# Optimization experiments

Hardware: AMD Instinct MI355X
Metric: run time of the kernel (lower is better)

The kernel has to match this reference:

```python
import jax, jax.numpy as jnp
import numpy as np

B, O, N = 8, 100, 4096
TOK_D, D, K, H = 2048, 256, 128, 8
DH = D // H
LN_EPS = 1e-5


def _ln(x, g, b):
    m = x.mean(-1, keepdims=True)
    v = ((x - m) ** 2).mean(-1, keepdims=True)
    return (x - m) * jax.lax.rsqrt(v + LN_EPS) * g + b


def setup_inputs() -> dict:
    key = jax.random.key(0)
    ks = jax.random.split(key, 16)
    s = 0.02
    return {
        "activation": jax.random.uniform(ks[0], (B, O, N), jnp.float32),
        "tokens": jax.random.normal(ks[1], (B, N, TOK_D), jnp.float32),
        "W_tok": jax.random.normal(ks[2], (TOK_D, D), jnp.float32) * s,
        "b_tok": jnp.zeros((D,), jnp.float32),
        "g_tn": jnp.ones((D,), jnp.float32),
        "bt_tn": jnp.zeros((D,), jnp.float32),
        "pool_query": jax.random.normal(ks[3], (D,), jnp.float32) * s,
        "Wq": jax.random.normal(ks[4], (D, D), jnp.float32) * s,
        "bq": jnp.zeros((D,), jnp.float32),
        "Wk": jax.random.normal(ks[5], (D, D), jnp.float32) * s,
        "bk": jnp.zeros((D,), jnp.float32),
        "Wv": jax.random.normal(ks[6], (D, D), jnp.float32) * s,
        "bv": jnp.zeros((D,), jnp.float32),
        "Wo": jax.random.normal(ks[7], (D, D), jnp.float32) * s,
        "bo": jnp.zeros((D,), jnp.float32),
        "g_pn": jnp.ones((D,), jnp.float32),
        "bt_pn": jnp.zeros((D,), jnp.float32),
        "g_on": jnp.ones((D,), jnp.float32),
        "bt_on": jnp.zeros((D,), jnp.float32),
    }


def reference(activation, tokens, W_tok, b_tok, g_tn, bt_tn, pool_query,
              Wq, bq, Wk, bk, Wv, bv, Wo, bo, g_pn, bt_pn, g_on, bt_on):
    # project + norm the shared token pool: [B, N, D]
    tp = _ln(tokens @ W_tok + b_tok, g_tn, bt_tn)

    # weighted-average branch
    w = activation / jnp.clip(activation.sum(-1, keepdims=True), 1e-8)
    weighted_avg = jnp.einsum('bon,bnd->bod', w, tp)

    # top-k attention branch
    _, topk_idx = jax.lax.top_k(activation, K)            # [B, O, K]
    topk_tokens = jax.vmap(lambda t, i: t[i])(tp, topk_idx)  # [B, O, K, D]

    # MultiheadAttention with a single shared query vector (q_len = 1)
    q = (pool_query @ Wq + bq).reshape(H, DH)             # [H, DH]
    kp = (topk_tokens @ Wk + bk).reshape(B, O, K, H, DH)
    vp = (topk_tokens @ Wv + bv).reshape(B, O, K, H, DH)
    scores = jnp.einsum('hd,bokhd->bohk', q, kp) / np.sqrt(DH).astype(np.float32)
    attn = jax.nn.softmax(scores, axis=-1)                # [B, O, H, K]
    pooled = jnp.einsum('bohk,bokhd->bohd', attn, vp).reshape(B, O, D)
    pooled = _ln(pooled @ Wo + bo, g_pn, bt_pn)

    return _ln(weighted_avg + pooled, g_on, bt_on)
```

## Files before the change

### kernel.cpp

```cpp
#include <hip/hip_runtime.h>
#include <hip/hip_bf16.h>

#define DEVI static __device__ __forceinline__

typedef __attribute__((ext_vector_type(8))) short short8;
typedef __attribute__((ext_vector_type(4))) float f32x4;

#define B_   8
#define O_   100
#define N_   4096
#define TOKD 2048
#define D_   256
#define K_   128
#define H_   8
#define M_   (B_*N_)

DEVI unsigned short f2bf(float f) {
    unsigned u = __float_as_uint(f);
    u = (u + 0x7FFFu + ((u >> 16) & 1u)) >> 16;
    return (unsigned short)u;
}
DEVI float bf2f(unsigned v) { return __uint_as_float(v << 16); }

DEVI unsigned pkbf(float lo, float hi) {
    unsigned r;
    asm("v_cvt_pk_bf16_f32 %0, %1, %2" : "=v"(r) : "v"(lo), "v"(hi));
    return r;
}
DEVI void gload16(const void* g, void* l) {
    __builtin_amdgcn_global_load_lds((const __attribute__((address_space(1))) void*)g,
                                     (__attribute__((address_space(3))) void*)l, 16, 0, 0);
}

__global__ __launch_bounds__(256) void k_trans(const float* __restrict__ W,
                                               unsigned short* __restrict__ wtb) {
    __shared__ unsigned short ldsT[32 * 264];
    const int t = threadIdx.x;
    const int k0 = (blockIdx.x >> 3) * 256;
    const int n0 = (blockIdx.x & 7) * 32;
    const int nn = t & 31, kk8 = t >> 5;
    #pragma unroll
    for (int r = 0; r < 32; ++r) {
        int k = r * 8 + kk8;
        ldsT[nn * 264 + k] = f2bf(W[(size_t)(k0 + k) * D_ + n0 + nn]);
    }
    __syncthreads();
    const int w = t >> 6, l = t & 63;
    #pragma unroll
    for (int rr = 0; rr < 8; ++rr) {
        int n = w * 8 + rr;
        ushort4 v = *(const ushort4*)(&ldsT[n * 264 + l * 4]);
        *(ushort4*)(wtb + (size_t)(n0 + n) * TOKD + k0 + l * 4) = v;
    }
}

__global__ __launch_bounds__(256) void k_topkqf(const float* __restrict__ act,
                                                int* __restrict__ oidx,
                                                float* __restrict__ asum,
                                                const float* __restrict__ pq,
                                                const float* __restrict__ Wq,
                                                const float* __restrict__ bqv,
                                                const float* __restrict__ Wk,
                                                const float* __restrict__ bkv,
                                                float* __restrict__ qW,
                                                float* __restrict__ qb) {
    __shared__ __align__(16) char smem[50304];
    const int t = threadIdx.x, lane = t & 63, wid = t >> 6;

    if (blockIdx.x >= 800) {
        float (*qpart)[32] = (float(*)[32])smem;
        float* qhl = (float*)(smem + 1024);
        const int h = blockIdx.x - 800;
        const int col = h * 32 + (t & 31), sl = t >> 5;
        float s = 0.f;
        #pragma unroll
        for (int e = 0; e < 32; ++e) s += pq[sl * 32 + e] * Wq[(sl * 32 + e) * D_ + col];
        qpart[sl][t & 31] = s;
        __syncthreads();
        if (t < 32) {
            float u = bqv[h * 32 + t];
            #pragma unroll
            for (int s8 = 0; s8 < 8; ++s8) u += qpart[s8][t];
            qhl[t] = u;
        }
        __syncthreads();
        float u = 0.f;
        #pragma unroll
        for (int dd = 0; dd < 32; ++dd) u += qhl[dd] * Wk[t * D_ + h * 32 + dd];
        qW[h * D_ + t] = u;
        if (t == 0) {
            float z = 0.f;
            for (int dd = 0; dd < 32; ++dd) z += qhl[dd] * bkv[h * 32 + dd];
            qb[h] = z;
        }
        return;
    }

    int* hist = (int*)smem;
    unsigned long long* cand = (unsigned long long*)(smem + 16384);
    int* csum = (int*)(smem + 49152);
    int* sb   = (int*)(smem + 50192);
    int* cnts = (int*)(smem + 50200);
    float* redf = (float*)(smem + 50208);
    unsigned long long* redu = (unsigned long long*)(smem + 50224);

    const int blk = blockIdx.x;
    const float* rp = act + (size_t)blk * N_;
    float fv[16]; unsigned vb[16]; int bins[16];
    float fs = 0.f;
    #pragma unroll
    for (int i = 0; i < 16; ++i) {
        float f = rp[t + i * 256];
        fv[i] = f; vb[i] = __float_as_uint(f);
        fs += f;
    }
    #pragma unroll
    for (int i = 0; i < 16; ++i) hist[t + i * 256] = 0;
    if (t == 0) { cnts[0] = 0; cnts[1] = 0; }
    #pragma unroll
    for (int m = 1; m < 64; m <<= 1) fs += __shfl_xor(fs, m);
    if (!lane) redf[wid] = fs;
    __syncthreads();
    if (t == 0) asum[blk] = fmaxf(redf[0] + redf[1] + redf[2] + redf[3], 1e-8f);

    #pragma unroll
    for (int i = 0; i < 16; ++i) {
        float f = fv[i];
        int b = (f >= 1.0f) ? 4095 : ((f > 0.f) ? (int)(f * 4096.f) : 0);
        bins[i] = b;
        atomicAdd(&hist[b], 1);
    }
    __syncthreads();

    int cs = 0;
    #pragma unroll
    for (int i = 0; i < 16; ++i) cs += hist[t * 16 + i];
    int v = cs;
    #pragma unroll
    for (int off = 1; off < 64; off <<= 1) {
        int o = __shfl_down(v, off);
        if (lane + off < 64) v += o;
    }
    if (!lane) csum[256 + wid] = v;
    __syncthreads();
    int stot = 0;
    for (int w2 = wid + 1; w2 < 4; ++w2) stot += csum[256 + w2];
    int suff = v + stot;
    csum[t] = suff;
    __syncthreads();
    int nxtc = (t < 255) ? csum[t + 1] : 0;
    if (suff >= K_ && nxtc < K_) {
        int run = nxtc, bstar = t * 16;
        for (int bi = 15; bi >= 0; --bi) {
            run += hist[t * 16 + bi];
            if (run >= K_) { bstar = t * 16 + bi; break; }
        }
        sb[0] = bstar;
    }
    __syncthreads();
    const int bstar = sb[0];

    #pragma unroll
    for (int i = 0; i < 16; ++i) {
        if (bins[i] > bstar) {
            int p = atomicAdd(&cnts[0], 1);
            oidx[blk * K_ + p] = t + i * 256;
        } else if (bins[i] == bstar) {
            int p = atomicAdd(&cnts[1], 1);
            cand[p] = ((unsigned long long)vb[i] << 16) | (unsigned)(4095 - (t + i * 256));
        }
    }
    __syncthreads();
    const int g = cnts[0], E = cnts[1], m = K_ - g;
    unsigned long long last = ~0ull;
    for (int slot = 0; slot < m; ++slot) {
        unsigned long long best = 0;
        for (int i = t; i < E; i += 256) {
            unsigned long long e = cand[i];
            if (e < last && e > best) best = e;
        }
        #pragma unroll
        for (int mm = 1; mm < 64; mm <<= 1) {
            unsigned long long o = __shfl_xor(best, mm);
            if (o > best) best = o;
        }
        if (!lane) redu[wid] = best;
        __syncthreads();
        best = redu[0];
        if (redu[1] > best) best = redu[1];
        if (redu[2] > best) best = redu[2];
        if (redu[3] > best) best = redu[3];
        if (t == 0) oidx[blk * K_ + g + slot] = 4095 - (int)(best & 0xFFFFull);
        last = best;
        __syncthreads();
    }
}

__global__ __launch_bounds__(512, 2) void k_gemm1(const float* __restrict__ A,
                                                  const unsigned short* __restrict__ Bt,
                                                  const float* __restrict__ btok,
                                                  const float* __restrict__ g,
                                                  const float* __restrict__ bt,
                                                  unsigned short* __restrict__ tp) {
    __shared__ __align__(16) char smem[81920];
    const int t = threadIdx.x;
    const int bm = blockIdx.x;
    const int lane = t & 63, w = t >> 6;
    const int wm = w >> 2, wn = w & 3;
    const int lr = lane >> 4, lc = lane & 15;

    const int arow = t >> 3;
    const int acb = (t & 7) * 16;
    const float* agp = A + (size_t)(bm * 64 + arow) * TOKD + (t & 7) * 8;
    const int aw0 = arow * 128 + (acb ^ ((arow & 7) << 4));
    const unsigned short* bg = Bt + (size_t)(t >> 3) * TOKD
                        + (((((t & 7) << 4)) ^ (((t >> 3) & 7) << 4)) >> 1);
    char* bld = smem + 16384 + (w << 10);

    f32x4 acc[2][4] = {};
    const int NT = TOKD / 64;
    float4 a0, a1;

    a0 = *(const float4*)(agp); a1 = *(const float4*)(agp + 4);
    #pragma unroll
    for (int c = 0; c < 4; ++c) gload16(bg + (size_t)c * 64 * TOKD, bld + c * 8192);
    {
        uint4 v;
        v.x = pkbf(a0.x, a0.y); v.y = pkbf(a0.z, a0.w);
        v.z = pkbf(a1.x, a1.y); v.w = pkbf(a1.z, a1.w);
        *(uint4*)(smem + aw0) = v;
    }
    a0 = *(const float4*)(agp + 64); a1 = *(const float4*)(agp + 68);
    asm volatile("s_waitcnt vmcnt(2) lgkmcnt(0)" ::: "memory");
    __builtin_amdgcn_s_barrier();

    int cur = 0;
    for (int kt = 0; kt < NT; ++kt) {
        const int nxt = cur ^ 1;
        if (kt + 1 < NT) {
            const unsigned short* bn = bg + (size_t)(kt + 1) * 64;
            char* dst = bld + nxt * 32768;
            #pragma unroll
            for (int c = 0; c < 4; ++c) gload16(bn + (size_t)c * 64 * TOKD, dst + c * 8192);
        }
        const char* Ab = smem + cur * 8192;
        const char* Bb = smem + 16384 + cur * 32768;
        #pragma unroll
        for (int kk = 0; kk < 2; ++kk) {
            short8 afr[2], bfr[4];
            #pragma unroll
            for (int mi = 0; mi < 2; ++mi) {
                int row = wm * 32 + mi * 16 + lc;
                afr[mi] = *(const short8*)(Ab + row * 128 + ((kk * 64 + lr * 16) ^ ((row & 7) << 4)));
            }
            #pragma unroll
            for (int ni = 0; ni < 4; ++ni) {
                int n = wn * 64 + ni * 16 + lc;
                bfr[ni] = *(const short8*)(Bb + n * 128 + ((kk * 64 + lr * 16) ^ ((n & 7) << 4)));
            }
            __builtin_amdgcn_s_setprio(1);
            #pragma unroll
            for (int mi = 0; mi < 2; ++mi)
                #pragma unroll
                for (int ni = 0; ni < 4; ++ni)
                    acc[mi][ni] = __builtin_amdgcn_mfma_f32_16x16x32_bf16(afr[mi], bfr[ni], acc[mi][ni], 0, 0, 0);
            __builtin_amdgcn_s_setprio(0);
        }
        if (kt + 1 < NT) {
            uint4 v;
            v.x = pkbf(a0.x, a0.y); v.y = pkbf(a0.z, a0.w);
            v.z = pkbf(a1.x, a1.y); v.w = pkbf(a1.z, a1.w);
            *(uint4*)(smem + nxt * 8192 + aw0) = v;
            if (kt + 2 < NT) {
                const float* ap = agp + (size_t)(kt + 2) * 64;
                a0 = *(const float4*)(ap); a1 = *(const float4*)(ap + 4);
                asm volatile("s_waitcnt vmcnt(2) lgkmcnt(0)" ::: "memory");
            } else {
                asm volatile("s_waitcnt vmcnt(0) lgkmcnt(0)" ::: "memory");
            }
            __builtin_amdgcn_s_barrier();
            cur = nxt;
        }
    }
    __syncthreads();

    float* ep = (float*)smem;
    const int col0 = lane * 4;
    float4 b4 = *(const float4*)(btok + col0);
    float4 g4 = *(const float4*)(g + col0);
    float4 t4 = *(const float4*)(bt + col0);
    #pragma unroll
    for (int c = 0; c < 2; ++c) {
        if (wm == c) {
            #pragma unroll
            for (int mi = 0; mi < 2; ++mi)
                #pragma unroll
                for (int ni = 0; ni < 4; ++ni)
                    #pragma unroll
                    for (int r = 0; r < 4; ++r)
                        ep[(mi * 16 + lr * 4 + r) * 260 + wn * 64 + ni * 16 + lc] = acc[mi][ni][r];
        }
        __syncthreads();
        #pragma unroll
        for (int rr = 0; rr < 4; ++rr) {
            int row = w * 4 + rr;
            float4 x4 = *(const float4*)(ep + row * 260 + col0);
            float x0 = x4.x + b4.x, x1 = x4.y + b4.y, x2 = x4.z + b4.z, x3 = x4.w + b4.w;
            float s = x0 + x1 + x2 + x3;
            float q = x0*x0 + x1*x1 + x2*x2 + x3*x3;
            #pragma unroll
            for (int m = 1; m < 64; m <<= 1) { s += __shfl_xor(s, m); q += __shfl_xor(q, m); }
            float mean = s * (1.f/256.f);
            float var = q * (1.f/256.f) - mean * mean;
            float rs = rsqrtf(var + 1e-5f);
            ushort4 o;
            o.x = f2bf((x0-mean)*rs*g4.x + t4.x);
            o.y = f2bf((x1-mean)*rs*g4.y + t4.y);
            o.z = f2bf((x2-mean)*rs*g4.z + t4.z);
            o.w = f2bf((x3-mean)*rs*g4.w + t4.w);
            *(ushort4*)(tp + (size_t)(bm * 64 + c * 32 + row) * D_ + col0) = o;
        }
        __syncthreads();
    }
}

__global__ __launch_bounds__(256) void k_wavg(const float* __restrict__ act,
                                              const unsigned short* __restrict__ tp,
                                              float* __restrict__ partial) {
    const int kc = blockIdx.x;
    const int b = blockIdx.y;
    const int d = threadIdx.x;
    const unsigned short* tpb = tp + ((size_t)b * N_ + kc * 128) * D_ + d;
    const float* actb = act + (size_t)b * O_ * N_ + kc * 128;
    float* pout = partial + ((size_t)(b * 32 + kc) * O_) * D_ + d;
    for (int oci = 0; oci < 2; ++oci) {
        const int oc = blockIdx.z * 2 + oci;
        float acc[10] = {};
        #pragma unroll 2
        for (int q = 0; q < 32; ++q) {
            float t0 = bf2f(tpb[(q * 4 + 0) * D_]);
            float t1 = bf2f(tpb[(q * 4 + 1) * D_]);
            float t2 = bf2f(tpb[(q * 4 + 2) * D_]);
            float t3 = bf2f(tpb[(q * 4 + 3) * D_]);
            #pragma unroll
            for (int oj = 0; oj < 10; ++oj) {
                float4 a4 = *(const float4*)(actb + (size_t)(oc * 10 + oj) * N_ + q * 4);
                acc[oj] += a4.x * t0 + a4.y * t1 + a4.z * t2 + a4.w * t3;
            }
        }
        #pragma unroll
        for (int oj = 0; oj < 10; ++oj)
            pout[(size_t)(oc * 10 + oj) * D_] = acc[oj];
    }
}

DEVI int swz64(int j, int chunk) { return j * 512 + ((chunk ^ (j & 31)) << 4); }

__global__ __launch_bounds__(256) void k_attn(
    const unsigned short* __restrict__ tp, const int* __restrict__ oidx,
    const float* __restrict__ qW, const float* __restrict__ qbv,
    const float* __restrict__ Wv, const float* __restrict__ bv,
    const float* __restrict__ Wo, const float* __restrict__ bo,
    const float* __restrict__ g_pn, const float* __restrict__ bt_pn,
    const float* __restrict__ g_on, const float* __restrict__ bt_on,
    const float* __restrict__ partial, const float* __restrict__ asum,
    float* __restrict__ outp)
{
    __shared__ __align__(16) char tg[32768];
    __shared__ float sc[H_ * K_];
    __shared__ float redf[8];
    __shared__ int idxl[K_];
    float* ul = (float*)tg;
    float* pool_lds = (float*)(tg + 8192);

    const int t = threadIdx.x, lane = t & 63, wid = t >> 6;
    const int blk = blockIdx.x;
    const int b = blk / O_;
    const int o = blk - b * O_;

    if (t < K_) idxl[t] = oidx[blk * K_ + t];
    __syncthreads();

    const int jq = t & 63, hp = t >> 6;
    const float* qr0 = qW + (hp * 2) * D_;
    const float* qr1 = qr0 + D_;
    const float sca = 0.1767766952966369f;

    for (int pass = 0; pass < 2; ++pass) {
        #pragma unroll
        for (int it = 0; it < 8; ++it) {
            int c = t + it * 256;
            int j = c >> 5, ch = c & 31;
            uint4 v = *(const uint4*)(tp + ((size_t)(b * N_ + idxl[pass * 64 + j])) * D_ + ch * 8);
            *(uint4*)(tg + swz64(j, ch)) = v;
        }
        __syncthreads();
        float s0 = 0.f, s1 = 0.f;
        #pragma unroll 4
        for (int e8 = 0; e8 < 32; ++e8) {
            uint4 tv = *(const uint4*)(tg + swz64(jq, e8));
            float f0 = bf2f(tv.x & 0xffffu), f1 = bf2f(tv.x >> 16);
            float f2 = bf2f(tv.y & 0xffffu), f3 = bf2f(tv.y >> 16);
            float f4 = bf2f(tv.z & 0xffffu), f5 = bf2f(tv.z >> 16);
            float f6 = bf2f(tv.w & 0xffffu), f7 = bf2f(tv.w >> 16);
            const float* qa = qr0 + e8 * 8;
            const float* qc = qr1 + e8 * 8;
            s0 += f0*qa[0]+f1*qa[1]+f2*qa[2]+f3*qa[3]+f4*qa[4]+f5*qa[5]+f6*qa[6]+f7*qa[7];
            s1 += f0*qc[0]+f1*qc[1]+f2*qc[2]+f3*qc[3]+f4*qc[4]+f5*qc[5]+f6*qc[6]+f7*qc[7];
        }
        sc[(hp * 2)     * K_ + pass * 64 + jq] = (s0 + qbv[hp * 2])     * sca;
        sc[(hp * 2 + 1) * K_ + pass * 64 + jq] = (s1 + qbv[hp * 2 + 1]) * sca;
        __syncthreads();
    }

    #pragma unroll
    for (int hh = 0; hh < 2; ++hh) {
        int h = wid * 2 + hh;
        float v0 = sc[h * K_ + lane], v1 = sc[h * K_ + 64 + lane];
        float mx = fmaxf(v0, v1);
        #pragma unroll
        for (int m = 1; m < 64; m <<= 1) mx = fmaxf(mx, __shfl_xor(mx, m));
        float e0 = __expf(v0 - mx), e1 = __expf(v1 - mx);
        float ss = e0 + e1;
        #pragma unroll
        for (int m = 1; m < 64; m <<= 1) ss += __shfl_xor(ss, m);
        float inv = 1.0f / ss;
        sc[h * K_ + lane] = e0 * inv;
        sc[h * K_ + 64 + lane] = e1 * inv;
    }
    __syncthreads();

    const int hq5 = t >> 5, eg = t & 31;
    float a8[8] = {};
    #pragma unroll 2
    for (int jb = 0; jb < 16; ++jb) {
        f32x4 p4 = *(const f32x4*)(sc + hq5 * K_ + 64 + jb * 4);
        #pragma unroll
        for (int ji = 0; ji < 4; ++ji) {
            int j = jb * 4 + ji;
            uint4 tv = *(const uint4*)(tg + swz64(j, eg));
            float pw = p4[ji];
            a8[0] += pw * bf2f(tv.x & 0xffffu); a8[1] += pw * bf2f(tv.x >> 16);
            a8[2] += pw * bf2f(tv.y & 0xffffu); a8[3] += pw * bf2f(tv.y >> 16);
            a8[4] += pw * bf2f(tv.z & 0xffffu); a8[5] += pw * bf2f(tv.z >> 16);
            a8[6] += pw * bf2f(tv.w & 0xffffu); a8[7] += pw * bf2f(tv.w >> 16);
        }
    }
    __syncthreads();
    #pragma unroll
    for (int it = 0; it < 8; ++it) {
        int c = t + it * 256;
        int j = c >> 5, ch = c & 31;
        uint4 v = *(const uint4*)(tp + ((size_t)(b * N_ + idxl[j])) * D_ + ch * 8);
        *(uint4*)(tg + swz64(j, ch)) = v;
    }
    __syncthreads();
    #pragma unroll 2
    for (int jb = 0; jb < 16; ++jb) {
        f32x4 p4 = *(const f32x4*)(sc + hq5 * K_ + jb * 4);
        #pragma unroll
        for (int ji = 0; ji < 4; ++ji) {
            int j = jb * 4 + ji;
            uint4 tv = *(const uint4*)(tg + swz64(j, eg));
            float pw = p4[ji];
            a8[0] += pw * bf2f(tv.x & 0xffffu); a8[1] += pw * bf2f(tv.x >> 16);
            a8[2] += pw * bf2f(tv.y & 0xffffu); a8[3] += pw * bf2f(tv.y >> 16);
            a8[4] += pw * bf2f(tv.z & 0xffffu); a8[5] += pw * bf2f(tv.z >> 16);
            a8[6] += pw * bf2f(tv.w & 0xffffu); a8[7] += pw * bf2f(tv.w >> 16);
        }
    }
    __syncthreads();
    #pragma unroll
    for (int i = 0; i < 8; ++i) ul[hq5 * D_ + eg * 8 + i] = a8[i];
    __syncthreads();

    {
        int h = t >> 5;
        const float* up = ul + h * D_;
        float p0 = 0.f, p1 = 0.f, p2 = 0.f, p3 = 0.f;
        #pragma unroll 4
        for (int e = 0; e < 64; ++e) {
            p0 += up[e]       * Wv[(size_t)e         * D_ + t];
            p1 += up[e + 64]  * Wv[(size_t)(e + 64)  * D_ + t];
            p2 += up[e + 128] * Wv[(size_t)(e + 128) * D_ + t];
            p3 += up[e + 192] * Wv[(size_t)(e + 192) * D_ + t];
        }
        pool_lds[t] = bv[t] + ((p0 + p1) + (p2 + p3));
    }
    __syncthreads();
    float po;
    {
        float p0 = 0.f, p1 = 0.f, p2 = 0.f, p3 = 0.f;
        #pragma unroll 4
        for (int e = 0; e < 64; ++e) {
            p0 += pool_lds[e]       * Wo[(size_t)e         * D_ + t];
            p1 += pool_lds[e + 64]  * Wo[(size_t)(e + 64)  * D_ + t];
            p2 += pool_lds[e + 128] * Wo[(size_t)(e + 128) * D_ + t];
            p3 += pool_lds[e + 192] * Wo[(size_t)(e + 192) * D_ + t];
        }
        po = bo[t] + ((p0 + p1) + (p2 + p3));
    }

    float lsm = po, lqm = po * po;
    #pragma unroll
    for (int m = 1; m < 64; m <<= 1) { lsm += __shfl_xor(lsm, m); lqm += __shfl_xor(lqm, m); }
    if (!lane) { redf[wid] = lsm; redf[4 + wid] = lqm; }
    __syncthreads();
    lsm = redf[0] + redf[1] + redf[2] + redf[3];
    lqm = redf[4] + redf[5] + redf[6] + redf[7];
    float mean = lsm * (1.f/256.f);
    float var = lqm * (1.f/256.f) - mean * mean;
    float rs = rsqrtf(var + 1e-5f);
    float pl = (po - mean) * rs * g_pn[t] + bt_pn[t];
    __syncthreads();

    float wa = 0.f;
    const float* pp = partial + ((size_t)(b * 32) * O_ + o) * D_ + t;
    #pragma unroll 8
    for (int kc = 0; kc < 32; ++kc) wa += pp[(size_t)kc * O_ * D_];
    float x = wa / asum[blk] + pl;
    float s2 = x, q2 = x * x;
    #pragma unroll
    for (int m = 1; m < 64; m <<= 1) { s2 += __shfl_xor(s2, m); q2 += __shfl_xor(q2, m); }
    if (!lane) { redf[wid] = s2; redf[4 + wid] = q2; }
    __syncthreads();
    s2 = redf[0] + redf[1] + redf[2] + redf[3];
    q2 = redf[4] + redf[5] + redf[6] + redf[7];
    float mean2 = s2 * (1.f/256.f);
    float var2 = q2 * (1.f/256.f) - mean2 * mean2;
    float rs2 = rsqrtf(var2 + 1e-5f);
    outp[(size_t)blk * D_ + t] = (x - mean2) * rs2 * g_on[t] + bt_on[t];
}

extern "C" void kernel_launch(void* const* d_in, const int* in_sizes, int n_in,
                              void* d_out, int out_size, void* d_ws, size_t ws_size,
                              hipStream_t stream) {
    const float* act    = (const float*)d_in[0];
    const float* tokens = (const float*)d_in[1];
    const float* W_tok  = (const float*)d_in[2];
    const float* b_tok  = (const float*)d_in[3];
    const float* g_tn   = (const float*)d_in[4];
    const float* bt_tn  = (const float*)d_in[5];
    const float* pq     = (const float*)d_in[6];
    const float* Wq     = (const float*)d_in[7];
    const float* bq     = (const float*)d_in[8];
    const float* Wk     = (const float*)d_in[9];
    const float* bk     = (const float*)d_in[10];
    const float* Wv     = (const float*)d_in[11];
    const float* bv     = (const float*)d_in[12];
    const float* Wo     = (const float*)d_in[13];
    const float* bo     = (const float*)d_in[14];
    const float* g_pn   = (const float*)d_in[15];
    const float* bt_pn  = (const float*)d_in[16];
    const float* g_on   = (const float*)d_in[17];
    const float* bt_on  = (const float*)d_in[18];

    char* ws = (char*)d_ws;
    unsigned short* wtb   = (unsigned short*)ws;
    unsigned short* tp    = (unsigned short*)(ws + 1048576);
    int*   tidx = (int*)(ws + 17825792);
    float* asum = (float*)(ws + 18235392);
    float* part = (float*)(ws + 18238592);
    float* qW   = (float*)(ws + 44452992);
    float* qb   = (float*)(ws + 44461184);

    k_trans<<<64, 256, 0, stream>>>(W_tok, wtb);
    k_gemm1<<<M_ / 64, 512, 0, stream>>>(tokens, wtb, b_tok, g_tn, bt_tn, tp);
    k_wavg<<<dim3(32, 8, 5), 256, 0, stream>>>(act, tp, part);
    k_topkqf<<<808, 256, 0, stream>>>(act, tidx, asum, pq, Wq, bq, Wk, bk, qW, qb);
    k_attn<<<B_ * O_, 256, 0, stream>>>(tp, tidx, qW, qb, Wv, bv, Wo, bo,
                                        g_pn, bt_pn, g_on, bt_on, part, asum,
                                        (float*)d_out);
}
```

Measured before the change: 219.5 us.

## Shrink token-projection GEMM tile to 32 rows with register-staged loads

The token projection GEMM now uses 32-row M tiles, a K step of 32 and padded unswizzled LDS, so it needs less shared memory and can run more blocks per CU. The direct global-to-LDS loads of W are replaced with register-staged uint4 loads, and only half the threads load A. This targets latency hiding through occupancy and a larger grid. In exchange, each block reuses the full 256-column B tile over fewer rows, so B traffic from L2 doubles and there are twice as many barriers per K.

```diff
diff --git a/kernel.cpp b/kernel.cpp
--- a/kernel.cpp
+++ b/kernel.cpp
@@ -26,10 +26,6 @@
     unsigned r;
     asm("v_cvt_pk_bf16_f32 %0, %1, %2" : "=v"(r) : "v"(lo), "v"(hi));
     return r;
-}
-DEVI void gload16(const void* g, void* l) {
-    __builtin_amdgcn_global_load_lds((const __attribute__((address_space(1))) void*)g,
-                                     (__attribute__((address_space(3))) void*)l, 16, 0, 0);
 }
 
 __global__ __launch_bounds__(256) void k_trans(const float* __restrict__ W,
@@ -196,90 +192,75 @@
     }
 }
 
-__global__ __launch_bounds__(512, 2) void k_gemm1(const float* __restrict__ A,
+__global__ __launch_bounds__(512, 4) void k_gemm1(const float* __restrict__ A,
                                                   const unsigned short* __restrict__ Bt,
                                                   const float* __restrict__ btok,
                                                   const float* __restrict__ g,
                                                   const float* __restrict__ bt,
                                                   unsigned short* __restrict__ tp) {
-    __shared__ __align__(16) char smem[81920];
+    __shared__ __align__(16) char smem[46080];
     const int t = threadIdx.x;
     const int bm = blockIdx.x;
     const int lane = t & 63, w = t >> 6;
     const int wm = w >> 2, wn = w & 3;
     const int lr = lane >> 4, lc = lane & 15;
-
-    const int arow = t >> 3;
-    const int acb = (t & 7) * 16;
-    const float* agp = A + (size_t)(bm * 64 + arow) * TOKD + (t & 7) * 8;
-    const int aw0 = arow * 128 + (acb ^ ((arow & 7) << 4));
-    const unsigned short* bg = Bt + (size_t)(t >> 3) * TOKD
-                        + (((((t & 7) << 4)) ^ (((t >> 3) & 7) << 4)) >> 1);
-    char* bld = smem + 16384 + (w << 10);
-
-    f32x4 acc[2][4] = {};
-    const int NT = TOKD / 64;
-    float4 a0, a1;
-
-    a0 = *(const float4*)(agp); a1 = *(const float4*)(agp + 4);
-    #pragma unroll
-    for (int c = 0; c < 4; ++c) gload16(bg + (size_t)c * 64 * TOKD, bld + c * 8192);
-    {
-        uint4 v;
-        v.x = pkbf(a0.x, a0.y); v.y = pkbf(a0.z, a0.w);
-        v.z = pkbf(a1.x, a1.y); v.w = pkbf(a1.z, a1.w);
-        *(uint4*)(smem + aw0) = v;
-    }
-    a0 = *(const float4*)(agp + 64); a1 = *(const float4*)(agp + 68);
-    asm volatile("s_waitcnt vmcnt(2) lgkmcnt(0)" ::: "memory");
-    __builtin_amdgcn_s_barrier();
-
-    int cur = 0;
+    const int NT = TOKD / 32;
+
+    const bool ast = (t < 256);
+    const float* agp = A + (size_t)(bm * 32 + ((t >> 3) & 31)) * TOKD + (t & 7) * 4;
+    const int awo = (t >> 3) * 80 + (t & 7) * 8;
+    const unsigned short* bgp = Bt + (size_t)(t >> 1) * TOKD + (t & 1) * 16;
+    const int bwo = (t >> 1) * 80 + (t & 1) * 32;
+    const int aro = (wm * 16 + lc) * 80 + lr * 16;
+    const int bro = (wn * 64 + lc) * 80 + lr * 16;
+
+    f32x4 acc[4] = {};
+    float4 ta = {0.f, 0.f, 0.f, 0.f};
+    uint4 tb0, tb1;
+
+    if (ast) ta = *(const float4*)(agp);
+    tb0 = *(const uint4*)(bgp);
+    tb1 = *(const uint4*)(bgp + 8);
+    if (ast) {
+        uint2 v; v.x = pkbf(ta.x, ta.y); v.y = pkbf(ta.z, ta.w);
+        *(uint2*)(smem + awo) = v;
+    }
+    *(uint4*)(smem + 5120 + bwo) = tb0;
+    *(uint4*)(smem + 5120 + bwo + 16) = tb1;
+    if (ast) ta = *(const float4*)(agp + 32);
+    tb0 = *(const uint4*)(bgp + 32);
+    tb1 = *(const uint4*)(bgp + 40);
+    __syncthreads();
+
     for (int kt = 0; kt < NT; ++kt) {
-        const int nxt = cur ^ 1;
+        const int cur = kt & 1, nxt = cur ^ 1;
+        const char* Ab = smem + cur * 2560;
+        const char* Bb = smem + 5120 + cur * 20480;
+        short8 afr = *(const short8*)(Ab + aro);
+        short8 bfr0 = *(const short8*)(Bb + bro);
+        short8 bfr1 = *(const short8*)(Bb + bro + 16 * 80);
+        short8 bfr2 = *(const short8*)(Bb + bro + 32 * 80);
+        short8 bfr3 = *(const short8*)(Bb + bro + 48 * 80);
+        __builtin_amdgcn_s_setprio(1);
+        acc[0] = __builtin_amdgcn_mfma_f32_16x16x32_bf16(afr, bfr0, acc[0], 0, 0, 0);
+        acc[1] = __builtin_amdgcn_mfma_f32_16x16x32_bf16(afr, bfr1, acc[1], 0, 0, 0);
+        acc[2] = __builtin_amdgcn_mfma_f32_16x16x32_bf16(afr, bfr2, acc[2], 0, 0, 0);
+        acc[3] = __builtin_amdgcn_mfma_f32_16x16x32_bf16(afr, bfr3, acc[3], 0, 0, 0);
+        __builtin_amdgcn_s_setprio(0);
         if (kt + 1 < NT) {
-            const unsigned short* bn = bg + (size_t)(kt + 1) * 64;
-            char* dst = bld + nxt * 32768;
-            #pragma unroll
-            for (int c = 0; c < 4; ++c) gload16(bn + (size_t)c * 64 * TOKD, dst + c * 8192);
-        }
-        const char* Ab = smem + cur * 8192;
-        const char* Bb = smem + 16384 + cur * 32768;
-        #pragma unroll
-        for (int kk = 0; kk < 2; ++kk) {
-            short8 afr[2], bfr[4];
-            #pragma unroll
-            for (int mi = 0; mi < 2; ++mi) {
-                int row = wm * 32 + mi * 16 + lc;
-                afr[mi] = *(const short8*)(Ab + row * 128 + ((kk * 64 + lr * 16) ^ ((row & 7) << 4)));
+            if (ast) {
+                uint2 v; v.x = pkbf(ta.x, ta.y); v.y = pkbf(ta.z, ta.w);
+                *(uint2*)(smem + nxt * 2560 + awo) = v;
             }
-            #pragma unroll
-            for (int ni = 0; ni < 4; ++ni) {
-                int n = wn * 64 + ni * 16 + lc;
-                bfr[ni] = *(const short8*)(Bb + n * 128 + ((kk * 64 + lr * 16) ^ ((n & 7) << 4)));
+            *(uint4*)(smem + 5120 + nxt * 20480 + bwo) = tb0;
+            *(uint4*)(smem + 5120 + nxt * 20480 + bwo + 16) = tb1;
+            if (kt + 2 < NT) {
+                if (ast) ta = *(const float4*)(agp + (kt + 2) * 32);
+                tb0 = *(const uint4*)(bgp + (kt + 2) * 32);
+                tb1 = *(const uint4*)(bgp + (kt + 2) * 32 + 8);
             }
-            __builtin_amdgcn_s_setprio(1);
-            #pragma unroll
-            for (int mi = 0; mi < 2; ++mi)
-                #pragma unroll
-                for (int ni = 0; ni < 4; ++ni)
-                    acc[mi][ni] = __builtin_amdgcn_mfma_f32_16x16x32_bf16(afr[mi], bfr[ni], acc[mi][ni], 0, 0, 0);
-            __builtin_amdgcn_s_setprio(0);
-        }
-        if (kt + 1 < NT) {
-            uint4 v;
-            v.x = pkbf(a0.x, a0.y); v.y = pkbf(a0.z, a0.w);
-            v.z = pkbf(a1.x, a1.y); v.w = pkbf(a1.z, a1.w);
-            *(uint4*)(smem + nxt * 8192 + aw0) = v;
-            if (kt + 2 < NT) {
-                const float* ap = agp + (size_t)(kt + 2) * 64;
-                a0 = *(const float4*)(ap); a1 = *(const float4*)(ap + 4);
-                asm volatile("s_waitcnt vmcnt(2) lgkmcnt(0)" ::: "memory");
-            } else {
-                asm volatile("s_waitcnt vmcnt(0) lgkmcnt(0)" ::: "memory");
-            }
+            asm volatile("s_waitcnt lgkmcnt(0)" ::: "memory");
             __builtin_amdgcn_s_barrier();
-            cur = nxt;
         }
     }
     __syncthreads();
@@ -290,37 +271,29 @@
     float4 g4 = *(const float4*)(g + col0);
     float4 t4 = *(const float4*)(bt + col0);
     #pragma unroll
-    for (int c = 0; c < 2; ++c) {
-        if (wm == c) {
-            #pragma unroll
-            for (int mi = 0; mi < 2; ++mi)
-                #pragma unroll
-                for (int ni = 0; ni < 4; ++ni)
-                    #pragma unroll
-                    for (int r = 0; r < 4; ++r)
-                        ep[(mi * 16 + lr * 4 + r) * 260 + wn * 64 + ni * 16 + lc] = acc[mi][ni][r];
-        }
-        __syncthreads();
-        #pragma unroll
-        for (int rr = 0; rr < 4; ++rr) {
-            int row = w * 4 + rr;
-            float4 x4 = *(const float4*)(ep + row * 260 + col0);
-            float x0 = x4.x + b4.x, x1 = x4.y + b4.y, x2 = x4.z + b4.z, x3 = x4.w + b4.w;
-            float s = x0 + x1 + x2 + x3;
-            float q = x0*x0 + x1*x1 + x2*x2 + x3*x3;
-            #pragma unroll
-            for (int m = 1; m < 64; m <<= 1) { s += __shfl_xor(s, m); q += __shfl_xor(q, m); }
-            float mean = s * (1.f/256.f);
-            float var = q * (1.f/256.f) - mean * mean;
-            float rs = rsqrtf(var + 1e-5f);
-            ushort4 o;
-            o.x = f2bf((x0-mean)*rs*g4.x + t4.x);
-            o.y = f2bf((x1-mean)*rs*g4.y + t4.y);
-            o.z = f2bf((x2-mean)*rs*g4.z + t4.z);
-            o.w = f2bf((x3-mean)*rs*g4.w + t4.w);
-            *(ushort4*)(tp + (size_t)(bm * 64 + c * 32 + row) * D_ + col0) = o;
-        }
-        __syncthreads();
+    for (int ni = 0; ni < 4; ++ni)
+        #pragma unroll
+        for (int r = 0; r < 4; ++r)
+            ep[(wm * 16 + lr * 4 + r) * 260 + wn * 64 + ni * 16 + lc] = acc[ni][r];
+    __syncthreads();
+    #pragma unroll
+    for (int rr = 0; rr < 4; ++rr) {
+        int row = w * 4 + rr;
+        float4 x4 = *(const float4*)(ep + row * 260 + col0);
+        float x0 = x4.x + b4.x, x1 = x4.y + b4.y, x2 = x4.z + b4.z, x3 = x4.w + b4.w;
+        float s = x0 + x1 + x2 + x3;
+        float q = x0*x0 + x1*x1 + x2*x2 + x3*x3;
+        #pragma unroll
+        for (int m = 1; m < 64; m <<= 1) { s += __shfl_xor(s, m); q += __shfl_xor(q, m); }
+        float mean = s * (1.f/256.f);
+        float var = q * (1.f/256.f) - mean * mean;
+        float rs = rsqrtf(var + 1e-5f);
+        ushort4 o;
+        o.x = f2bf((x0-mean)*rs*g4.x + t4.x);
+        o.y = f2bf((x1-mean)*rs*g4.y + t4.y);
+        o.z = f2bf((x2-mean)*rs*g4.z + t4.z);
+        o.w = f2bf((x3-mean)*rs*g4.w + t4.w);
+        *(ushort4*)(tp + (size_t)(bm * 32 + row) * D_ + col0) = o;
     }
 }
 
@@ -565,7 +538,7 @@
     float* qb   = (float*)(ws + 44461184);
 
     k_trans<<<64, 256, 0, stream>>>(W_tok, wtb);
-    k_gemm1<<<M_ / 64, 512, 0, stream>>>(tokens, wtb, b_tok, g_tn, bt_tn, tp);
+    k_gemm1<<<M_ / 32, 512, 0, stream>>>(tokens, wtb, b_tok, g_tn, bt_tn, tp);
     k_wavg<<<dim3(32, 8, 5), 256, 0, stream>>>(act, tp, part);
     k_topkqf<<<808, 256, 0, stream>>>(act, tidx, asum, pq, Wq, bq, Wk, bk, qW, qb);
     k_attn<<<B_ * O_, 256, 0, stream>>>(tp, tidx, qW, qb, Wv, bv, Wo, bo,
```

Measured after the change: 294.9 us. +34.4%, slower.
